# Kernel tuning notes

Hardware: AMD Instinct MI355X
Metric: run time of the kernel (lower is better)

Reference implementation:

```python
import jax, jax.numpy as jnp
import numpy as np

T, N, NN = 16, 64, 32          # ob_T, agents, neighbors
D, H, DK, DFF, L = 512, 8, 64, 2048, 2
NUM_PRED, OB_R = 20, 2.0


def _w(k, shape):
    fan_in = shape[-2] if len(shape) > 1 else shape[-1]
    return jax.random.normal(k, shape, jnp.float32) / np.sqrt(fan_in).astype(np.float32)


def setup_inputs():
    key = jax.random.key(0)
    ks = jax.random.split(key, 16)
    return {
        "x": jax.random.normal(ks[0], (T, N, 6), jnp.float32),
        "neighbor": jax.random.normal(ks[1], (T, N, NN, 4), jnp.float32),
        "att_factor": jax.random.uniform(ks[2], (1,), jnp.float32),
        "Wx": _w(ks[3], (4, D)), "bx": jnp.zeros((D,), jnp.float32),
        "Wn": _w(ks[4], (3, D)), "bn": jnp.zeros((D,), jnp.float32),
        "Wpred": _w(ks[5], (D, 2)), "bpred": jnp.zeros((2,), jnp.float32),
        "WQ": _w(ks[6], (L, D, H * DK)),
        "WK": _w(ks[7], (L, D, H * DK)),
        "WV": _w(ks[8], (L, D, H * DK)),
        "Wfc": _w(ks[9], (L, H * DK, D)),
        "mha_ln_g": jnp.ones((L, D), jnp.float32), "mha_ln_b": jnp.zeros((L, D), jnp.float32),
        "WSI": _w(ks[10], (L, H * D, D)),
        "ffs_w1": _w(ks[11], (L, D, DFF)), "ffs_w2": _w(ks[12], (L, DFF, D)),
        "ffs_ln_g": jnp.ones((L, D), jnp.float32), "ffs_ln_b": jnp.zeros((L, D), jnp.float32),
        "ffi_w1": _w(ks[13], (L, D, DFF)), "ffi_w2": _w(ks[14], (L, DFF, D)),
        "ffi_ln_g": jnp.ones((L, D), jnp.float32), "ffi_ln_b": jnp.zeros((L, D), jnp.float32),
    }


def _ln(x, g, b, eps=1e-5):
    m = x.mean(-1, keepdims=True)
    v = x.var(-1, keepdims=True)
    return (x - m) / jnp.sqrt(v + eps) * g + b


def reference(x, neighbor, att_factor, Wx, bx, Wn, bn, Wpred, bpred,
              WQ, WK, WV, Wfc, mha_ln_g, mha_ln_b, WSI,
              ffs_w1, ffs_w2, ffs_ln_g, ffs_ln_b,
              ffi_w1, ffi_w2, ffi_ln_g, ffi_ln_b):
    # ---- trajectory features ----
    velocity = jnp.linalg.norm(x[:, :, 2:4], axis=-1, keepdims=True)
    v_angle = jnp.arctan(x[:, :, 5] / x[:, :, 4])[..., None]
    x_f = jnp.nan_to_num(jnp.concatenate([x[:, :, 0:2], velocity, v_angle], axis=-1))
    pos = x[..., :2]                                       # [T,N,2]
    v = jnp.concatenate([x[1:2, ..., 2:4], pos[1:] - pos[:-1]], axis=0)  # [T,N,2]
    dp = neighbor[..., :2] - pos[:, :, None, :]            # [T,N,Nn,2]
    dv = neighbor[..., 2:4] - v[:, :, None, :]
    dist = jnp.linalg.norm(dp, axis=-1)                    # [T,N,Nn]
    mask = (dist <= OB_R).transpose(1, 2, 0)               # [N,Nn,T] (query-time mask)
    dot_dp_v = jnp.einsum('tnmd,tnd->tnm', dp, v)
    bearing = dot_dp_v / (dist * jnp.linalg.norm(v, axis=-1)[:, :, None])
    bearing = jnp.where(jnp.isnan(bearing), 0.0, bearing)
    dot_dp_dv = jnp.einsum('tnmd,tnmd->tnm', dp, dv)
    tau = -dot_dp_dv / jnp.linalg.norm(dv, axis=-1)
    tau = jnp.clip(jnp.where(jnp.isnan(tau), 0.0, tau), 0.0, 7.0)
    mpd = jnp.linalg.norm(dp + tau[..., None] * dv, axis=-1)
    neighbor_f = jnp.nan_to_num(jnp.stack([dist, bearing, mpd], axis=-1))  # [T,N,Nn,3]

    # ---- positional encoding (note: pos * 10000^(2i/d), as in the source) ----
    position = jnp.arange(T, dtype=jnp.float32)[:, None]
    div = jnp.power(10000.0, jnp.arange(0, D, 2, dtype=jnp.float32) / D)
    pe = jnp.zeros((T, D), jnp.float32)
    pe = pe.at[:, 0::2].set(jnp.sin(position * div)).at[:, 1::2].set(jnp.cos(position * div))

    x_emb = (x_f @ Wx + bx) + pe[:, None, :]               # [T,N,D]
    n_emb = (neighbor_f @ Wn + bn) + pe[:, None, None, :]  # [T,N,Nn,D]
    x_emb = x_emb.transpose(1, 0, 2)                       # [N,T,D]
    n_emb = n_emb.transpose(1, 2, 0, 3)                    # [N,Nn,T,D]

    amask = mask[:, :, None, :, None]   # [N,Nn,1(heads),T(query),1(key)]
    factor = att_factor[0]
    sk = 1.0 / np.sqrt(DK).astype(np.float32)
    sd = 1.0 / np.sqrt(D).astype(np.float32)

    for l in range(L):
        # --- masked MHA over the time axis, per (agent, neighbor) ---
        q = (n_emb @ WQ[l]).reshape(N, NN, T, H, DK).transpose(0, 1, 3, 2, 4)
        k = (n_emb @ WK[l]).reshape(N, NN, T, H, DK).transpose(0, 1, 3, 2, 4)
        vv = (n_emb @ WV[l]).reshape(N, NN, T, H, DK).transpose(0, 1, 3, 2, 4)
        scores = jnp.einsum('bmhqd,bmhkd->bmhqk', q, k) * sk
        scores = jnp.where(amask, scores, -1e9)
        attn = jax.nn.softmax(scores, axis=-1)             # [N,Nn,H,T,T]
        ctx = jnp.einsum('bmhqk,bmhkd->bmhqd', attn, vv)
        ctx = ctx.transpose(0, 1, 3, 2, 4).reshape(N, NN, T, H * DK)
        res_inter = _ln(ctx @ Wfc[l] + n_emb, mha_ln_g[l], mha_ln_b[l])

        # --- self/inter attention fusion ---
        att_inter = attn.mean(axis=1)                      # [N,H,T,T]
        att_self = jax.nn.softmax(jnp.einsum('nqd,nkd->nqk', x_emb, x_emb) * sd, axis=-1)
        att = att_self[:, None, :, :] + factor * att_inter # [N,H,T,T]
        si = jnp.einsum('nhqt,ntd->nqhd', att, x_emb).reshape(N, T, H * D)
        x_new = si @ WSI[l]                                # [N,T,D]

        # --- FFN + LayerNorm (self and inter branches) ---
        x_emb = _ln(jax.nn.relu(x_new @ ffs_w1[l]) @ ffs_w2[l] + x_new,
                    ffs_ln_g[l], ffs_ln_b[l])
        n_emb = _ln(jax.nn.relu(res_inter @ ffi_w1[l]) @ ffi_w2[l] + res_inter,
                    ffi_ln_g[l], ffi_ln_b[l])

    out = x_emb @ Wpred + bpred                            # [N,T,2]
    out = jnp.broadcast_to(out[None], (NUM_PRED, N, T, 2)).transpose(0, 2, 1, 3)
    return out                                             # [20,T,N,2]
```

## Files before the change

kernel.cpp:

```cpp
#include <hip/hip_runtime.h>
#include <math.h>


#define T_ 16
#define N_ 64
#define NN_ 32
#define D_ 512
#define H_ 8
#define DK_ 64
#define DFF_ 2048
#define L_ 2
#define NPRED_ 20

typedef unsigned short u16;
typedef unsigned int u32;
typedef __attribute__((ext_vector_type(8))) short short8;
typedef __attribute__((ext_vector_type(4))) float f32x4;

__device__ __forceinline__ u16 f2bf(float f) {
    u32 u = __float_as_uint(f);
    u32 r = u + 0x7fffu + ((u >> 16) & 1u);
    return (u16)(r >> 16);
}
__device__ __forceinline__ float bfv(u16 v) {
    return __uint_as_float(((u32)v) << 16);
}
__device__ __forceinline__ float ntn(float v) {
    if (isnan(v)) return 0.0f;
    if (isinf(v)) return v > 0.0f ? 3.4028234663852886e38f : -3.4028234663852886e38f;
    return v;
}
__device__ __forceinline__ float wave_sum(float v) {
    #pragma unroll
    for (int o = 32; o > 0; o >>= 1) v += __shfl_xor(v, o, 64);
    return v;
}
__device__ __forceinline__ void gload_lds(const u16* g, u16* l) {
    __builtin_amdgcn_global_load_lds(
        (const __attribute__((address_space(1))) u32*)g,
        (__attribute__((address_space(3))) u32*)l, 16, 0, 0);
}

struct WJob { const float* src; u16* dst; int K; int N; int t0; };
struct WJobs { WJob j[14]; };
__global__ __launch_bounds__(256) void wconv_all(WJobs jobs, int ntiles) {
    int bid = blockIdx.x;
    if (bid >= ntiles) return;
    int ji = 0;
    #pragma unroll 1
    for (int i = 1; i < 14; ++i) if (bid >= jobs.j[i].t0) ji = i;
    const float* in = jobs.j[ji].src;
    u16* out = jobs.j[ji].dst;
    int K = jobs.j[ji].K, N = jobs.j[ji].N;
    int lt = bid - jobs.j[ji].t0;
    int ntx = N >> 5;
    int nb = (lt % ntx) * 32, kb = (lt / ntx) * 32;
    __shared__ float tile[32][33];
    int tx = threadIdx.x & 31, ty = threadIdx.x >> 5;
    #pragma unroll
    for (int r = ty; r < 32; r += 8)
        tile[r][tx] = in[(size_t)(kb + r) * N + nb + tx];
    __syncthreads();
    #pragma unroll
    for (int r = ty; r < 32; r += 8)
        out[(size_t)(nb + r) * K + kb + tx] = f2bf(tile[tx][r]);
}

template<int TM, int TN, int EPI, int WF32, int WBF16>
__global__ __launch_bounds__(256) void gemm_bt(
    const u16* __restrict__ Ab, const u16* __restrict__ Btb,
    float* __restrict__ Cf, u16* __restrict__ Cb, const void* __restrict__ Rg,
    int K, int ldc)
{
    constexpr int WR = TM / 32, WC = TN / 32;
    constexpr int ITA = TM / 32, ITB = TN / 32;
    __shared__ __align__(16) u16 As[TM][64];
    __shared__ __align__(16) u16 Bs[TN][64];
    int tid = threadIdx.x;
    int lane = tid & 63, wave = tid >> 6;
    int quad = lane >> 4, l16 = lane & 15;
    int wm = (wave >> 1) * (TM / 2), wn = (wave & 1) * (TN / 2);

    int gx = gridDim.x, gy = gridDim.y;
    int bx, by;
    if ((gy & 7) == 0) {
        int id = blockIdx.y * gx + blockIdx.x;
        int xcd = id & 7;
        int slot = id >> 3;
        bx = slot % gx;
        by = xcd * (gy >> 3) + slot / gx;
    } else {
        bx = blockIdx.x;
        by = blockIdx.y;
    }
    size_t row0 = (size_t)by * TM;
    size_t col0 = (size_t)bx * TN;

    f32x4 acc[WR][WC];
    #pragma unroll
    for (int i = 0; i < WR; ++i)
        #pragma unroll
        for (int j = 0; j < WC; ++j)
            acc[i][j] = (f32x4){0.f, 0.f, 0.f, 0.f};

    int srow = lane >> 3;
    int c8 = (lane & 7) ^ srow;
    int h8 = l16 & 7;

    for (int k0 = 0; k0 < K; k0 += 64) {
        __syncthreads();
        #pragma unroll
        for (int it = 0; it < ITA; ++it) {
            int g = wave + it * 4;
            gload_lds(Ab + (row0 + g * 8 + srow) * (size_t)K + k0 + c8 * 8, &As[g * 8][0]);
        }
        #pragma unroll
        for (int it = 0; it < ITB; ++it) {
            int g = wave + it * 4;
            gload_lds(Btb + (col0 + g * 8 + srow) * (size_t)K + k0 + c8 * 8, &Bs[g * 8][0]);
        }
        __syncthreads();
        #pragma unroll
        for (int s = 0; s < 2; ++s) {
            int coff = ((s * 4 + quad) ^ h8) * 8;
            short8 af[WR], bf[WC];
            #pragma unroll
            for (int i = 0; i < WR; ++i)
                af[i] = *(short8*)&As[wm + i * 16 + l16][coff];
            #pragma unroll
            for (int j = 0; j < WC; ++j)
                bf[j] = *(short8*)&Bs[wn + j * 16 + l16][coff];
            #pragma unroll
            for (int i = 0; i < WR; ++i)
                #pragma unroll
                for (int j = 0; j < WC; ++j)
                    acc[i][j] = __builtin_amdgcn_mfma_f32_16x16x32_bf16(
                        af[i], bf[j], acc[i][j], 0, 0, 0);
        }
    }
    #pragma unroll
    for (int i = 0; i < WR; ++i)
        #pragma unroll
        for (int j = 0; j < WC; ++j)
            #pragma unroll
            for (int reg = 0; reg < 4; ++reg) {
                size_t row = row0 + wm + i * 16 + quad * 4 + reg;
                size_t col = col0 + wn + j * 16 + l16;
                float v = acc[i][j][reg];
                if (EPI == 2) v += ((const float*)Rg)[row * (size_t)ldc + col];
                if (EPI == 3) v += bfv(((const u16*)Rg)[row * (size_t)ldc + col]);
                if (EPI == 1) v = fmaxf(v, 0.f);
                if (WF32)  Cf[row * (size_t)ldc + col] = v;
                if (WBF16) Cb[row * (size_t)ldc + col] = f2bf(v);
            }
}

template<int CTX, int LD>
__global__ __launch_bounds__(256) void attn_fused_kernel(
    const u16* __restrict__ QKVb, const float* __restrict__ maskf, int bm0,
    float* __restrict__ att_sum, u16* __restrict__ ctxb)
{
    __shared__ __align__(16) u16 sQ[16][520];
    __shared__ __align__(16) u16 sK[16][520];
    __shared__ __align__(16) u16 sV[CTX ? 16 : 1][520];
    __shared__ float s_p[H_][16][17];
    int bm_l = blockIdx.x;
    int tid = threadIdx.x;
    int t = tid >> 4, ch = (tid & 15) * 32;
    const u16* base = QKVb + ((size_t)bm_l * T_ + t) * LD;
    #pragma unroll
    for (int c = 0; c < 4; ++c) {
        *(uint4*)&sQ[t][ch + c * 8] = *(const uint4*)(base + ch + c * 8);
        *(uint4*)&sK[t][ch + c * 8] = *(const uint4*)(base + 512 + ch + c * 8);
        if (CTX) *(uint4*)&sV[t][ch + c * 8] = *(const uint4*)(base + 1024 + ch + c * 8);
    }
    __syncthreads();

    int b = (bm0 + bm_l) >> 5;

    #pragma unroll
    for (int r = 0; r < 8; ++r) {
        int h = r;
        int q = (tid >> 4) & 15, k = tid & 15;
        const u32* qu = (const u32*)&sQ[q][0] + h * 32;
        const u32* ku = (const u32*)&sK[k][0] + h * 32;
        float acc = 0.f;
        #pragma unroll
        for (int j = 0; j < 32; ++j) {
            u32 a = qu[j], bb = ku[j];
            acc += bfv((u16)(a & 0xffff)) * bfv((u16)(bb & 0xffff));
            acc += bfv((u16)(a >> 16))    * bfv((u16)(bb >> 16));
        }
        acc *= 0.125f;
        if (maskf[(size_t)(bm0 + bm_l) * T_ + q] == 0.0f) acc = -1e9f;
        s_p[h][q][k] = acc;
    }
    __syncthreads();
    if (tid < 128) {
        int h = tid >> 4, q = tid & 15;
        float mx = -3.4e38f;
        #pragma unroll
        for (int kk = 0; kk < 16; ++kk) mx = fmaxf(mx, s_p[h][q][kk]);
        float e[16], s = 0.f;
        #pragma unroll
        for (int kk = 0; kk < 16; ++kk) { e[kk] = expf(s_p[h][q][kk] - mx); s += e[kk]; }
        float inv = 1.0f / s;
        #pragma unroll
        for (int kk = 0; kk < 16; ++kk) s_p[h][q][kk] = e[kk] * inv;
    }
    __syncthreads();
    #pragma unroll
    for (int r = 0; r < 8; ++r) {
        int h = r;
        int q = (tid >> 4) & 15, k = tid & 15;
        atomicAdd(&att_sum[(((size_t)b * H_ + h) * T_ + q) * T_ + k], s_p[h][q][k]);
    }
    if (CTX) {
        #pragma unroll
        for (int rep = 0; rep < 16; ++rep) {
            int i2 = rep * 256 + tid;
            int tt = i2 >> 8, c2 = i2 & 255;
            int h = c2 >> 5;
            const float* pr = &s_p[h][tt][0];
            float a0 = 0.f, a1 = 0.f;
            #pragma unroll
            for (int kk = 0; kk < 16; ++kk) {
                u32 vv = *((const u32*)&sV[kk][0] + c2);
                float p = pr[kk];
                a0 += p * bfv((u16)(vv & 0xffff));
                a1 += p * bfv((u16)(vv >> 16));
            }
            u32 o = (u32)f2bf(a0) | ((u32)f2bf(a1) << 16);
            *((u32*)(ctxb + ((size_t)bm_l * T_ + tt) * D_) + c2) = o;
        }
    }
}

__global__ __launch_bounds__(256) void siatt_kernel(
    const float* __restrict__ xemb, const float* __restrict__ att_sum,
    const float* __restrict__ attf, u16* __restrict__ sib)
{
    __shared__ float sX[16][516];
    __shared__ float sS[16][17];
    __shared__ float sA[16][17];
    int n = blockIdx.x >> 3, h = blockIdx.x & 7;
    int tid = threadIdx.x;
    int t = tid >> 4, ch = (tid & 15) * 32;
    const float* src = xemb + ((size_t)n * T_ + t) * D_;
    #pragma unroll
    for (int c = 0; c < 8; ++c)
        *(float4*)&sX[t][ch + c * 4] = *(const float4*)(src + ch + c * 4);
    __syncthreads();
    int q = tid >> 4, k = tid & 15;
    {
        float acc = 0.f;
        for (int d = 0; d < D_; ++d) acc += sX[q][d] * sX[k][d];
        sS[q][k] = acc * 0.04419417382415922f;
    }
    __syncthreads();
    if (tid < T_) {
        float mx = -3.4e38f;
        #pragma unroll
        for (int kk = 0; kk < 16; ++kk) mx = fmaxf(mx, sS[tid][kk]);
        float e[16], s = 0.f;
        #pragma unroll
        for (int kk = 0; kk < 16; ++kk) { e[kk] = expf(sS[tid][kk] - mx); s += e[kk]; }
        float inv = 1.0f / s;
        #pragma unroll
        for (int kk = 0; kk < 16; ++kk) sS[tid][kk] = e[kk] * inv;
    }
    __syncthreads();
    float f = attf[0] * (1.0f / 32.0f);
    sA[q][k] = sS[q][k] + f * att_sum[((size_t)n * H_ + h) * 256 + q * 16 + k];
    __syncthreads();
    #pragma unroll
    for (int rep = 0; rep < 16; ++rep) {
        int i2 = rep * 256 + tid;
        int qq = i2 >> 8, d2 = (i2 & 255) * 2;
        const float* ar = &sA[qq][0];
        float a0 = 0.f, a1 = 0.f;
        #pragma unroll
        for (int tt = 0; tt < 16; ++tt) {
            float p = ar[tt];
            a0 += p * sX[tt][d2];
            a1 += p * sX[tt][d2 + 1];
        }
        u32 o = (u32)f2bf(a0) | ((u32)f2bf(a1) << 16);
        *((u32*)(sib + (size_t)n * T_ * 4096 + (size_t)qq * 4096 + h * 512) + (d2 >> 1)) = o;
    }
}

__global__ void pe_kernel(float* pe) {
    int i = blockIdx.x * blockDim.x + threadIdx.x;
    if (i >= T_ * 256) return;
    int t = i >> 8, j = i & 255;
    float dv = (float)pow(10000.0, (double)j / 256.0);
    float a = (float)t * dv;
    double ad = (double)a;
    pe[t * D_ + 2 * j]     = (float)sin(ad);
    pe[t * D_ + 2 * j + 1] = (float)cos(ad);
}

__global__ void xemb_kernel(const float* x, const float* Wx, const float* bx,
                            const float* pe, float* xemb) {
    int row = blockIdx.x;
    int t = row / N_, n = row % N_;
    float x0 = x[row * 6 + 0], x1 = x[row * 6 + 1];
    float x2 = x[row * 6 + 2], x3 = x[row * 6 + 3];
    float x4 = x[row * 6 + 4], x5 = x[row * 6 + 5];
    float vel = sqrtf(x2 * x2 + x3 * x3);
    float ang = atanf(x5 / x4);
    float f0 = ntn(x0), f1 = ntn(x1), f2 = ntn(vel), f3 = ntn(ang);
    for (int d = threadIdx.x; d < D_; d += blockDim.x) {
        xemb[((size_t)n * T_ + t) * D_ + d] =
            f0 * Wx[0 * D_ + d] + f1 * Wx[1 * D_ + d]
          + f2 * Wx[2 * D_ + d] + f3 * Wx[3 * D_ + d]
          + bx[d] + pe[t * D_ + d];
    }
}

__global__ void nbr_kernel(const float* x, const float* nbr, float* nf, float* maskf) {
    int idx = blockIdx.x * blockDim.x + threadIdx.x;
    if (idx >= T_ * N_ * NN_) return;
    int m = idx % NN_;
    int tn = idx / NN_;
    int n = tn % N_, t = tn / N_;
    float px = x[((size_t)t * N_ + n) * 6 + 0];
    float py = x[((size_t)t * N_ + n) * 6 + 1];
    float vx, vy;
    if (t == 0) {
        vx = x[((size_t)1 * N_ + n) * 6 + 2];
        vy = x[((size_t)1 * N_ + n) * 6 + 3];
    } else {
        vx = px - x[((size_t)(t - 1) * N_ + n) * 6 + 0];
        vy = py - x[((size_t)(t - 1) * N_ + n) * 6 + 1];
    }
    float nx  = nbr[(size_t)idx * 4 + 0], ny  = nbr[(size_t)idx * 4 + 1];
    float nvx = nbr[(size_t)idx * 4 + 2], nvy = nbr[(size_t)idx * 4 + 3];
    float dpx = nx - px, dpy = ny - py;
    float dvx = nvx - vx, dvy = nvy - vy;
    float dist = sqrtf(dpx * dpx + dpy * dpy);
    maskf[((size_t)n * NN_ + m) * T_ + t] = (dist <= 2.0f) ? 1.0f : 0.0f;
    float vn = sqrtf(vx * vx + vy * vy);
    float bearing = (dpx * vx + dpy * vy) / (dist * vn);
    if (isnan(bearing)) bearing = 0.0f;
    float dvn = sqrtf(dvx * dvx + dvy * dvy);
    float tau = -(dpx * dvx + dpy * dvy) / dvn;
    if (isnan(tau)) tau = 0.0f;
    tau = fminf(fmaxf(tau, 0.0f), 7.0f);
    float mx_ = dpx + tau * dvx, my_ = dpy + tau * dvy;
    float mpd = sqrtf(mx_ * mx_ + my_ * my_);
    nf[(size_t)idx * 3 + 0] = ntn(dist);
    nf[(size_t)idx * 3 + 1] = ntn(bearing);
    nf[(size_t)idx * 3 + 2] = ntn(mpd);
}

__global__ void nemb_kernel(const float* nf, const float* Wn, const float* bn,
                            const float* pe, u16* Ab) {
    int row = blockIdx.x;
    int t = row % T_;
    int bm = row / T_;
    int m = bm % NN_, b = bm / NN_;
    size_t nfrow = (((size_t)t * N_ + b) * NN_ + m) * 3;
    float f0 = nf[nfrow], f1 = nf[nfrow + 1], f2 = nf[nfrow + 2];
    for (int d = threadIdx.x; d < D_; d += blockDim.x) {
        float v = f0 * Wn[d] + f1 * Wn[D_ + d] + f2 * Wn[2 * D_ + d]
                + bn[d] + pe[t * D_ + d];
        Ab[(size_t)row * D_ + d] = f2bf(v);
    }
}

template<int INBF>
__global__ __launch_bounds__(256) void ln_kernel(
    const void* X, const float* g, const float* b, float* outF, u16* outB, int nrows) {
    int row = blockIdx.x * 4 + (threadIdx.x >> 6);
    if (row >= nrows) return;
    int lane = threadIdx.x & 63;
    float v[8];
    float s = 0.f;
    #pragma unroll
    for (int r = 0; r < 8; ++r) {
        int d = lane + r * 64;
        v[r] = INBF ? bfv(((const u16*)X)[(size_t)row * D_ + d])
                    : ((const float*)X)[(size_t)row * D_ + d];
        s += v[r];
    }
    s = wave_sum(s);
    float mean = s * (1.0f / 512.0f);
    float vs = 0.f;
    #pragma unroll
    for (int r = 0; r < 8; ++r) { float d = v[r] - mean; vs += d * d; }
    vs = wave_sum(vs);
    float rstd = rsqrtf(vs * (1.0f / 512.0f) + 1e-5f);
    #pragma unroll
    for (int r = 0; r < 8; ++r) {
        int d = lane + r * 64;
        float o = (v[r] - mean) * rstd * g[d] + b[d];
        if (outF) outF[(size_t)row * D_ + d] = o;
        if (outB) outB[(size_t)row * D_ + d] = f2bf(o);
    }
}

__global__ void predbcast_kernel(const float* xemb, const float* Wp, const float* bp,
                                 float* out) {
    int idx = blockIdx.x * blockDim.x + threadIdx.x;
    if (idx >= N_ * T_ * 2) return;
    int c = idx & 1;
    int nt = idx >> 1;
    int n = nt / T_, t = nt % T_;
    float acc = bp[c];
    for (int j = 0; j < D_; ++j) acc += xemb[(size_t)nt * D_ + j] * Wp[(size_t)j * 2 + c];
    #pragma unroll
    for (int p = 0; p < NPRED_; ++p)
        out[(((size_t)p * T_ + t) * N_ + n) * 2 + c] = acc;
}

extern "C" void kernel_launch(void* const* d_in, const int* in_sizes, int n_in,
                              void* d_out, int out_size, void* d_ws, size_t ws_size,
                              hipStream_t stream) {
    (void)in_sizes; (void)n_in; (void)out_size; (void)ws_size;

    const float* x    = (const float*)d_in[0];
    const float* nbr  = (const float*)d_in[1];
    const float* attf = (const float*)d_in[2];
    const float* Wx   = (const float*)d_in[3];
    const float* bx   = (const float*)d_in[4];
    const float* Wn   = (const float*)d_in[5];
    const float* bn   = (const float*)d_in[6];
    const float* Wp   = (const float*)d_in[7];
    const float* bp   = (const float*)d_in[8];
    const float* WQ   = (const float*)d_in[9];
    const float* WK   = (const float*)d_in[10];
    const float* WV   = (const float*)d_in[11];
    const float* Wfc  = (const float*)d_in[12];
    const float* mlng = (const float*)d_in[13];
    const float* mlnb = (const float*)d_in[14];
    const float* WSI  = (const float*)d_in[15];
    const float* fsw1 = (const float*)d_in[16];
    const float* fsw2 = (const float*)d_in[17];
    const float* fsg  = (const float*)d_in[18];
    const float* fsb  = (const float*)d_in[19];
    const float* fiw1 = (const float*)d_in[20];
    const float* fiw2 = (const float*)d_in[21];
    const float* fig  = (const float*)d_in[22];
    const float* fib  = (const float*)d_in[23];

    char* w = (char*)d_ws;
    size_t off = 0;
    auto alloc = [&](size_t bytes) -> void* {
        void* p = w + off;
        off = (off + bytes + 255) & ~(size_t)255;
        return p;
    };
    const size_t MiB = 1024 * 1024;

    const int BM = N_ * NN_;
    const int ROWS_I = BM * T_;
    const int CB = 1024;
    const int RC = CB * T_;
    const int NCH = ROWS_I / RC;

    float* pe      = (float*)alloc((size_t)T_ * D_ * 4);
    float* xemb    = (float*)alloc((size_t)N_ * T_ * D_ * 4);
    float* nf      = (float*)alloc((size_t)T_ * N_ * NN_ * 3 * 4);
    float* maskf   = (float*)alloc((size_t)BM * T_ * 4);
    u16*   Ab      = (u16*)alloc((size_t)ROWS_I * D_ * 2);
    u16* tQKV[2], *tWSI[2], *tfs1[2], *tfs2[2];
    for (int l = 0; l < 2; ++l) {
        tQKV[l] = (u16*)alloc((size_t)1536 * 512 * 2);
        tWSI[l] = (u16*)alloc((size_t)512 * 4096 * 2);
        tfs1[l] = (u16*)alloc((size_t)2048 * 512 * 2);
        tfs2[l] = (u16*)alloc((size_t)512 * 2048 * 2);
    }
    u16* tWfc = (u16*)alloc((size_t)512 * 512 * 2);
    u16* tfi1 = (u16*)alloc((size_t)2048 * 512 * 2);
    u16* tfi2 = (u16*)alloc((size_t)512 * 2048 * 2);
    char* SCR  = (char*)alloc(64 * MiB);
    u16*   QKVb = (u16*)SCR;
    u16*   ctxb = (u16*)(SCR + 48 * MiB);
    u16*   hid  = (u16*)SCR;
    u16*   BbA    = (u16*)alloc((size_t)RC * D_ * 2);
    u16*   Bb_res = (u16*)alloc((size_t)RC * D_ * 2);
    float* att_sum = (float*)alloc((size_t)N_ * H_ * 256 * 4);
    u16*   sib     = (u16*)alloc((size_t)N_ * T_ * 4096 * 2);
    float* xnew    = (float*)alloc((size_t)N_ * T_ * D_ * 4);
    u16*   xnb     = (u16*)alloc((size_t)N_ * T_ * D_ * 2);

    WJobs jobs;
    int ntiles = 0;
    auto addJob = [&](int idx, const float* src, u16* dst, int K, int N) {
        jobs.j[idx] = {src, dst, K, N, ntiles};
        ntiles += (N >> 5) * (K >> 5);
    };
    addJob(0,  WQ,                            tQKV[0],              512, 512);
    addJob(1,  WK,                            tQKV[0] + 512 * 512,  512, 512);
    addJob(2,  WV,                            tQKV[0] + 1024 * 512, 512, 512);
    addJob(3,  WQ + (size_t)512 * 512,        tQKV[1],              512, 512);
    addJob(4,  WK + (size_t)512 * 512,        tQKV[1] + 512 * 512,  512, 512);
    addJob(5,  Wfc,                           tWfc,                 512, 512);
    addJob(6,  WSI,                           tWSI[0],              4096, 512);
    addJob(7,  WSI + (size_t)4096 * 512,      tWSI[1],              4096, 512);
    addJob(8,  fsw1,                          tfs1[0],              512, 2048);
    addJob(9,  fsw1 + (size_t)512 * 2048,     tfs1[1],              512, 2048);
    addJob(10, fsw2,                          tfs2[0],              2048, 512);
    addJob(11, fsw2 + (size_t)2048 * 512,     tfs2[1],              2048, 512);
    addJob(12, fiw1,                          tfi1,                 512, 2048);
    addJob(13, fiw2,                          tfi2,                 2048, 512);
    wconv_all<<<ntiles, 256, 0, stream>>>(jobs, ntiles);

    pe_kernel<<<16, 256, 0, stream>>>(pe);
    xemb_kernel<<<T_ * N_, 256, 0, stream>>>(x, Wx, bx, pe, xemb);
    nbr_kernel<<<(T_ * N_ * NN_ + 255) / 256, 256, 0, stream>>>(x, nbr, nf, maskf);
    nemb_kernel<<<BM * T_, 256, 0, stream>>>(nf, Wn, bn, pe, Ab);

    for (int l = 0; l < L_; ++l) {
        hipMemsetAsync(att_sum, 0, (size_t)N_ * H_ * 256 * 4, stream);
        if (l == 0) {
            for (int c = 0; c < NCH; ++c) {
                u16* Acb = Ab + (size_t)c * RC * D_;
                gemm_bt<128, 128, 0, 0, 1><<<dim3(12, RC / 128), 256, 0, stream>>>(
                    Acb, tQKV[0], nullptr, QKVb, nullptr, 512, 1536);
                attn_fused_kernel<1, 1536><<<CB, 256, 0, stream>>>(
                    QKVb, maskf, c * CB, att_sum, ctxb);
                gemm_bt<128, 128, 3, 0, 1><<<dim3(4, RC / 128), 256, 0, stream>>>(
                    ctxb, tWfc, nullptr, BbA, Acb, 512, 512);
                ln_kernel<1><<<RC / 4, 256, 0, stream>>>(
                    BbA, mlng, mlnb, nullptr, Bb_res, RC);
                gemm_bt<128, 128, 1, 0, 1><<<dim3(16, RC / 128), 256, 0, stream>>>(
                    Bb_res, tfi1, nullptr, hid, nullptr, 512, 2048);
                gemm_bt<128, 128, 3, 0, 1><<<dim3(4, RC / 128), 256, 0, stream>>>(
                    hid, tfi2, nullptr, BbA, Bb_res, 2048, 512);
                ln_kernel<1><<<RC / 4, 256, 0, stream>>>(
                    BbA, fig, fib, nullptr, Acb, RC);
            }
        } else {
            gemm_bt<128, 128, 0, 0, 1><<<dim3(8, ROWS_I / 128), 256, 0, stream>>>(
                Ab, tQKV[1], nullptr, QKVb, nullptr, 512, 1024);
            attn_fused_kernel<0, 1024><<<BM, 256, 0, stream>>>(
                QKVb, maskf, 0, att_sum, nullptr);
        }

        siatt_kernel<<<N_ * H_, 256, 0, stream>>>(xemb, att_sum, attf, sib);
        gemm_bt<32, 64, 0, 1, 1><<<dim3(8, 32), 256, 0, stream>>>(
            sib, tWSI[l], xnew, xnb, nullptr, 4096, 512);
        gemm_bt<32, 64, 1, 0, 1><<<dim3(32, 32), 256, 0, stream>>>(
            xnb, tfs1[l], nullptr, hid, nullptr, 512, 2048);
        gemm_bt<32, 64, 2, 1, 0><<<dim3(8, 32), 256, 0, stream>>>(
            hid, tfs2[l], xemb, nullptr, xnew, 2048, 512);
        ln_kernel<0><<<(N_ * T_) / 4, 256, 0, stream>>>(
            xemb, fsg + l * D_, fsb + l * D_, xemb, nullptr, N_ * T_);
    }

    predbcast_kernel<<<(N_ * T_ * 2 + 255) / 256, 256, 0, stream>>>(
        xemb, Wp, bp, (float*)d_out);
}
```

Before: 852.9 us.

## Add 256x256 double-buffered MFMA GEMM for large neighbor-branch matmuls

Adds a new 512-thread GEMM kernel with 256x256 output tiles, double-buffered LDS staging through direct global-to-LDS loads, XOR-swizzled LDS layout, wave priority hints and an XCD-aware block remapping. It replaces the 128x128 GEMMs used for the large neighbor-branch QKV, Wfc and FFN projections. Larger tiles cut global/L2 traffic per FLOP and overlap the next K tile's loads with MFMA work. In exchange it launches fewer blocks, which can reduce occupancy. The remap also assumes the grid's y dimension divides by 8.

```diff
diff --git a/kernel.cpp b/kernel.cpp
--- a/kernel.cpp
+++ b/kernel.cpp
@@ -142,6 +142,115 @@
     for (int i = 0; i < WR; ++i)
         #pragma unroll
         for (int j = 0; j < WC; ++j)
+            #pragma unroll
+            for (int reg = 0; reg < 4; ++reg) {
+                size_t row = row0 + wm + i * 16 + quad * 4 + reg;
+                size_t col = col0 + wn + j * 16 + l16;
+                float v = acc[i][j][reg];
+                if (EPI == 2) v += ((const float*)Rg)[row * (size_t)ldc + col];
+                if (EPI == 3) v += bfv(((const u16*)Rg)[row * (size_t)ldc + col]);
+                if (EPI == 1) v = fmaxf(v, 0.f);
+                if (WF32)  Cf[row * (size_t)ldc + col] = v;
+                if (WBF16) Cb[row * (size_t)ldc + col] = f2bf(v);
+            }
+}
+
+template<int EPI, int WF32, int WBF16>
+__global__ __launch_bounds__(512, 2) void gemm256_bt(
+    const u16* __restrict__ Ab, const u16* __restrict__ Btb,
+    float* __restrict__ Cf, u16* __restrict__ Cb, const void* __restrict__ Rg,
+    int K, int ldc)
+{
+    __shared__ __align__(16) u16 As[2][256][64];
+    __shared__ __align__(16) u16 Bs[2][256][64];
+    int tid = threadIdx.x;
+    int lane = tid & 63, wave = tid >> 6;
+    int quad = lane >> 4, l16 = lane & 15;
+    int wm = (wave >> 2) * 128, wn = (wave & 3) * 64;
+
+    int gx = gridDim.x, gy = gridDim.y;
+    int id = blockIdx.y * gx + blockIdx.x;
+    int xcd = id & 7, slot = id >> 3;
+    int bx = slot % gx;
+    int by = xcd * (gy >> 3) + slot / gx;
+    size_t row0 = (size_t)by * 256;
+    size_t col0 = (size_t)bx * 256;
+
+    f32x4 acc[8][4];
+    #pragma unroll
+    for (int i = 0; i < 8; ++i)
+        #pragma unroll
+        for (int j = 0; j < 4; ++j)
+            acc[i][j] = (f32x4){0.f, 0.f, 0.f, 0.f};
+
+    int srow = lane >> 3;
+    int c8 = (lane & 7) ^ srow;
+    int h8 = l16 & 7;
+
+    size_t aoff[4], boff[4];
+    #pragma unroll
+    for (int it = 0; it < 4; ++it) {
+        int g = wave + it * 8;
+        aoff[it] = (row0 + (size_t)g * 8 + srow) * (size_t)K + c8 * 8;
+        boff[it] = (col0 + (size_t)g * 8 + srow) * (size_t)K + c8 * 8;
+    }
+
+    #pragma unroll
+    for (int it = 0; it < 4; ++it)
+        gload_lds(Ab + aoff[it], &As[0][(wave + it * 8) * 8][0]);
+    #pragma unroll
+    for (int it = 0; it < 4; ++it)
+        gload_lds(Btb + boff[it], &Bs[0][(wave + it * 8) * 8][0]);
+    asm volatile("s_waitcnt vmcnt(0)" ::: "memory");
+    __builtin_amdgcn_s_barrier();
+
+    int nt = K >> 6;
+    #pragma unroll 1
+    for (int t = 0; t < nt; ++t) {
+        int cur = t & 1, nxt = cur ^ 1;
+        size_t knext = (size_t)(t + 1) * 64;
+        short8 af[4], bf[4];
+        #pragma unroll
+        for (int kh = 0; kh < 2; ++kh) {
+            #pragma unroll
+            for (int mh = 0; mh < 2; ++mh) {
+                int coff = ((kh * 4 + quad) ^ h8) * 8;
+                if (mh == 0) {
+                    #pragma unroll
+                    for (int j = 0; j < 4; ++j)
+                        bf[j] = *(short8*)&Bs[cur][wn + j * 16 + l16][coff];
+                }
+                #pragma unroll
+                for (int i = 0; i < 4; ++i)
+                    af[i] = *(short8*)&As[cur][wm + (mh * 4 + i) * 16 + l16][coff];
+                if (kh == 0 && mh == 0 && t + 1 < nt) {
+                    #pragma unroll
+                    for (int it = 0; it < 4; ++it)
+                        gload_lds(Ab + aoff[it] + knext, &As[nxt][(wave + it * 8) * 8][0]);
+                    #pragma unroll
+                    for (int it = 0; it < 4; ++it)
+                        gload_lds(Btb + boff[it] + knext, &Bs[nxt][(wave + it * 8) * 8][0]);
+                }
+                __builtin_amdgcn_s_barrier();
+                __builtin_amdgcn_s_setprio(1);
+                #pragma unroll
+                for (int i = 0; i < 4; ++i)
+                    #pragma unroll
+                    for (int j = 0; j < 4; ++j)
+                        acc[mh * 4 + i][j] = __builtin_amdgcn_mfma_f32_16x16x32_bf16(
+                            af[i], bf[j], acc[mh * 4 + i][j], 0, 0, 0);
+                __builtin_amdgcn_s_setprio(0);
+                __builtin_amdgcn_s_barrier();
+            }
+        }
+        asm volatile("s_waitcnt vmcnt(0)" ::: "memory");
+        __builtin_amdgcn_s_barrier();
+    }
+
+    #pragma unroll
+    for (int i = 0; i < 8; ++i)
+        #pragma unroll
+        for (int j = 0; j < 4; ++j)
             #pragma unroll
             for (int reg = 0; reg < 4; ++reg) {
                 size_t row = row0 + wm + i * 16 + quad * 4 + reg;
@@ -518,23 +627,23 @@
         if (l == 0) {
             for (int c = 0; c < NCH; ++c) {
                 u16* Acb = Ab + (size_t)c * RC * D_;
-                gemm_bt<128, 128, 0, 0, 1><<<dim3(12, RC / 128), 256, 0, stream>>>(
+                gemm256_bt<0, 0, 1><<<dim3(6, RC / 256), 512, 0, stream>>>(
                     Acb, tQKV[0], nullptr, QKVb, nullptr, 512, 1536);
                 attn_fused_kernel<1, 1536><<<CB, 256, 0, stream>>>(
                     QKVb, maskf, c * CB, att_sum, ctxb);
-                gemm_bt<128, 128, 3, 0, 1><<<dim3(4, RC / 128), 256, 0, stream>>>(
+                gemm256_bt<3, 0, 1><<<dim3(2, RC / 256), 512, 0, stream>>>(
                     ctxb, tWfc, nullptr, BbA, Acb, 512, 512);
                 ln_kernel<1><<<RC / 4, 256, 0, stream>>>(
                     BbA, mlng, mlnb, nullptr, Bb_res, RC);
-                gemm_bt<128, 128, 1, 0, 1><<<dim3(16, RC / 128), 256, 0, stream>>>(
+                gemm256_bt<1, 0, 1><<<dim3(8, RC / 256), 512, 0, stream>>>(
                     Bb_res, tfi1, nullptr, hid, nullptr, 512, 2048);
-                gemm_bt<128, 128, 3, 0, 1><<<dim3(4, RC / 128), 256, 0, stream>>>(
+                gemm256_bt<3, 0, 1><<<dim3(2, RC / 256), 512, 0, stream>>>(
                     hid, tfi2, nullptr, BbA, Bb_res, 2048, 512);
                 ln_kernel<1><<<RC / 4, 256, 0, stream>>>(
                     BbA, fig, fib, nullptr, Acb, RC);
             }
         } else {
-            gemm_bt<128, 128, 0, 0, 1><<<dim3(8, ROWS_I / 128), 256, 0, stream>>>(
+            gemm256_bt<0, 0, 1><<<dim3(4, ROWS_I / 256), 512, 0, stream>>>(
                 Ab, tQKV[1], nullptr, QKVb, nullptr, 512, 1024);
             attn_fused_kernel<0, 1024><<<BM, 256, 0, stream>>>(
                 QKVb, maskf, 0, att_sum, nullptr);
```

Result: slower. 913.2 us (+7.1%).

## Add 4-stage pipelined MFMA GEMM with swizzled LDS and XCD-aware tile mapping

Applied to the files above, without the earlier changes.

Adds a new bf16 MFMA GEMM kernel that prefetches three K-tiles ahead into a 4-deep LDS ring via direct global-to-LDS loads. It uses XOR-swizzled LDS addressing to avoid bank conflicts and remaps blocks so neighbouring tiles land on the same XCD. The large neighbor-branch GEMMs (QKV, FFN) now use this kernel with 256x256 tiles and 512 threads, and the smaller ones use 128x128. This targets memory latency stalls in the old GEMM, at the cost of more LDS, fewer resident blocks and a hand-written waitcnt that must match the number of loads in flight.

```diff
diff --git a/kernel.cpp b/kernel.cpp
--- a/kernel.cpp
+++ b/kernel.cpp
@@ -142,6 +142,124 @@
     for (int i = 0; i < WR; ++i)
         #pragma unroll
         for (int j = 0; j < WC; ++j)
+            #pragma unroll
+            for (int reg = 0; reg < 4; ++reg) {
+                size_t row = row0 + wm + i * 16 + quad * 4 + reg;
+                size_t col = col0 + wn + j * 16 + l16;
+                float v = acc[i][j][reg];
+                if (EPI == 2) v += ((const float*)Rg)[row * (size_t)ldc + col];
+                if (EPI == 3) v += bfv(((const u16*)Rg)[row * (size_t)ldc + col]);
+                if (EPI == 1) v = fmaxf(v, 0.f);
+                if (WF32)  Cf[row * (size_t)ldc + col] = v;
+                if (WBF16) Cb[row * (size_t)ldc + col] = f2bf(v);
+            }
+}
+
+template<int TM, int TN, int WMW, int WNW, int EPI, int WF32, int WBF16>
+__global__ __launch_bounds__(WMW * WNW * 64, 2) void gemm_p4(
+    const u16* __restrict__ Ab, const u16* __restrict__ Btb,
+    float* __restrict__ Cf, u16* __restrict__ Cb, const void* __restrict__ Rg,
+    int K, int ldc)
+{
+    constexpr int NW = WMW * WNW;
+    constexpr int FM = TM / WMW / 16;
+    constexpr int FN = TN / WNW / 16;
+    constexpr int CA = TM / 16 / NW;
+    constexpr int CBn = TN / 16 / NW;
+    __shared__ __align__(16) u16 As[4][TM][32];
+    __shared__ __align__(16) u16 Bs[4][TN][32];
+    int tid = threadIdx.x;
+    int lane = tid & 63, wave = tid >> 6;
+    int quad = lane >> 4, l16 = lane & 15;
+    int wm = (wave / WNW) * (FM * 16);
+    int wn = (wave % WNW) * (FN * 16);
+
+    int gx = gridDim.x, gy = gridDim.y;
+    int bx, by;
+    if ((gy & 7) == 0) {
+        int id = blockIdx.y * gx + blockIdx.x;
+        int xcd = id & 7, slot = id >> 3;
+        bx = slot % gx;
+        by = xcd * (gy >> 3) + slot / gx;
+    } else {
+        bx = blockIdx.x;
+        by = blockIdx.y;
+    }
+    size_t row0 = (size_t)by * TM;
+    size_t col0 = (size_t)bx * TN;
+
+    f32x4 acc[FM][FN];
+    #pragma unroll
+    for (int i = 0; i < FM; ++i)
+        #pragma unroll
+        for (int j = 0; j < FN; ++j)
+            acc[i][j] = (f32x4){0.f, 0.f, 0.f, 0.f};
+
+    int srow = lane >> 2;
+    int swz = (srow & 3) ^ (srow >> 2);
+    int sc = (lane & 3) ^ swz;
+    size_t aoff[CA], boff[CBn];
+    #pragma unroll
+    for (int it = 0; it < CA; ++it)
+        aoff[it] = (row0 + (size_t)(wave + it * NW) * 16 + srow) * (size_t)K + sc * 8;
+    #pragma unroll
+    for (int it = 0; it < CBn; ++it)
+        boff[it] = (col0 + (size_t)(wave + it * NW) * 16 + srow) * (size_t)K + sc * 8;
+
+    int gr = (l16 & 3) ^ (l16 >> 2);
+    int rc = (quad ^ gr) * 8;
+
+    int nt = K >> 5;
+    #pragma unroll
+    for (int pt = 0; pt < 3; ++pt) {
+        size_t ko = (size_t)pt * 32;
+        #pragma unroll
+        for (int it = 0; it < CA; ++it)
+            gload_lds(Ab + aoff[it] + ko, &As[pt][(wave + it * NW) * 16][0]);
+        #pragma unroll
+        for (int it = 0; it < CBn; ++it)
+            gload_lds(Btb + boff[it] + ko, &Bs[pt][(wave + it * NW) * 16][0]);
+    }
+
+    #pragma unroll 1
+    for (int t = 0; t < nt; ++t) {
+        int db = (t + 3) & 3;
+        size_t ko = (size_t)(t + 3 < nt ? t + 3 : 0) * 32;
+        #pragma unroll
+        for (int it = 0; it < CA; ++it)
+            gload_lds(Ab + aoff[it] + ko, &As[db][(wave + it * NW) * 16][0]);
+        #pragma unroll
+        for (int it = 0; it < CBn; ++it)
+            gload_lds(Btb + boff[it] + ko, &Bs[db][(wave + it * NW) * 16][0]);
+        __builtin_amdgcn_sched_barrier(0);
+        asm volatile("s_waitcnt vmcnt(12)" ::: "memory");
+        __builtin_amdgcn_sched_barrier(0);
+        __builtin_amdgcn_s_barrier();
+        __builtin_amdgcn_sched_barrier(0);
+        int buf = t & 3;
+        short8 af[FM], bf[FN];
+        #pragma unroll
+        for (int j = 0; j < FN; ++j)
+            bf[j] = *(short8*)&Bs[buf][wn + j * 16 + l16][rc];
+        #pragma unroll
+        for (int i = 0; i < FM; ++i)
+            af[i] = *(short8*)&As[buf][wm + i * 16 + l16][rc];
+        __builtin_amdgcn_s_setprio(1);
+        #pragma unroll
+        for (int i = 0; i < FM; ++i)
+            #pragma unroll
+            for (int j = 0; j < FN; ++j)
+                acc[i][j] = __builtin_amdgcn_mfma_f32_16x16x32_bf16(
+                    af[i], bf[j], acc[i][j], 0, 0, 0);
+        __builtin_amdgcn_s_setprio(0);
+        __builtin_amdgcn_sched_barrier(0);
+        __builtin_amdgcn_s_barrier();
+    }
+
+    #pragma unroll
+    for (int i = 0; i < FM; ++i)
+        #pragma unroll
+        for (int j = 0; j < FN; ++j)
             #pragma unroll
             for (int reg = 0; reg < 4; ++reg) {
                 size_t row = row0 + wm + i * 16 + quad * 4 + reg;
@@ -518,23 +636,23 @@
         if (l == 0) {
             for (int c = 0; c < NCH; ++c) {
                 u16* Acb = Ab + (size_t)c * RC * D_;
-                gemm_bt<128, 128, 0, 0, 1><<<dim3(12, RC / 128), 256, 0, stream>>>(
+                gemm_p4<256, 256, 2, 4, 0, 0, 1><<<dim3(6, RC / 256), 512, 0, stream>>>(
                     Acb, tQKV[0], nullptr, QKVb, nullptr, 512, 1536);
                 attn_fused_kernel<1, 1536><<<CB, 256, 0, stream>>>(
                     QKVb, maskf, c * CB, att_sum, ctxb);
-                gemm_bt<128, 128, 3, 0, 1><<<dim3(4, RC / 128), 256, 0, stream>>>(
+                gemm_p4<128, 128, 2, 2, 3, 0, 1><<<dim3(4, RC / 128), 256, 0, stream>>>(
                     ctxb, tWfc, nullptr, BbA, Acb, 512, 512);
                 ln_kernel<1><<<RC / 4, 256, 0, stream>>>(
                     BbA, mlng, mlnb, nullptr, Bb_res, RC);
-                gemm_bt<128, 128, 1, 0, 1><<<dim3(16, RC / 128), 256, 0, stream>>>(
+                gemm_p4<256, 256, 2, 4, 1, 0, 1><<<dim3(8, RC / 256), 512, 0, stream>>>(
                     Bb_res, tfi1, nullptr, hid, nullptr, 512, 2048);
-                gemm_bt<128, 128, 3, 0, 1><<<dim3(4, RC / 128), 256, 0, stream>>>(
+                gemm_p4<128, 128, 2, 2, 3, 0, 1><<<dim3(4, RC / 128), 256, 0, stream>>>(
                     hid, tfi2, nullptr, BbA, Bb_res, 2048, 512);
                 ln_kernel<1><<<RC / 4, 256, 0, stream>>>(
                     BbA, fig, fib, nullptr, Acb, RC);
             }
         } else {
-            gemm_bt<128, 128, 0, 0, 1><<<dim3(8, ROWS_I / 128), 256, 0, stream>>>(
+            gemm_p4<256, 256, 2, 4, 0, 0, 1><<<dim3(4, ROWS_I / 256), 512, 0, stream>>>(
                 Ab, tQKV[1], nullptr, QKVb, nullptr, 512, 1024);
             attn_fused_kernel<0, 1024><<<BM, 256, 0, stream>>>(
                 QKVb, maskf, 0, att_sum, nullptr);
```

Result: slower. 899.3 us (+5.4%).
